# Performance work log

Measured on AMD Instinct MI355X. Metric: run time of the kernel, lower is better.

The kernel has to match this reference:

```python
import jax, jax.numpy as jnp
import numpy as np
import math

F = 64        # num_features (multiplicity of each irrep)
N = 16000     # nodes
E = 256000    # edges (avg_num_neighbors = 16)
S = 4         # num_species
DE = 32       # scalar edge feature dim (radial basis)
W = 128       # interaction_mlp_width
AVG_NEIGH = 16.0
SQ2 = math.sqrt(2.0)
SQ3 = math.sqrt(3.0)


def setup_inputs() -> dict:
    key = jax.random.key(0)
    ks = jax.random.split(key, 32)
    def nrm(k, shape, scale=1.0):
        return jax.random.normal(k, shape, dtype=jnp.float32) * scale
    inp = {}
    # forward args
    inp["vectors"] = nrm(ks[0], (E, 1, 3))
    inp["lengths"] = jax.random.uniform(ks[1], (E, 1), dtype=jnp.float32)
    inp["node_s"] = nrm(ks[2], (N, F))            # 64x0e part of node_feats
    inp["node_v"] = nrm(ks[3], (N, F, 3))         # 64x1o part of node_feats
    inp["scalar_edge_feats"] = nrm(ks[4], (E, DE))
    inp["node_specie"] = jax.random.randint(ks[5], (N,), 0, S)
    inp["senders"] = jax.random.randint(ks[6], (E,), 0, N)
    inp["receivers"] = jax.random.randint(ks[7], (E,), 0, N)
    # parameters (e3nn Linear = per-irrep channel mixing, fan-in normalized; bias only on 0e)
    inp["W_up_s"] = nrm(ks[8], (F, F), F ** -0.5); inp["b_up_s"] = jnp.zeros((F,), jnp.float32)
    inp["W_up_v"] = nrm(ks[9], (F, F), F ** -0.5)
    din = 2 * F + DE + 1
    inp["mlp_W1"] = nrm(ks[10], (din, W), din ** -0.5); inp["mlp_b1"] = jnp.zeros((W,), jnp.float32)
    inp["mlp_W2"] = nrm(ks[11], (W, W), W ** -0.5); inp["mlp_b2"] = jnp.zeros((W,), jnp.float32)
    inp["mlp_W3"] = nrm(ks[12], (W, 3 * F), W ** -0.5); inp["mlp_b3"] = jnp.zeros((3 * F,), jnp.float32)
    inp["W_dn_s"] = nrm(ks[13], (F, F), F ** -0.5); inp["b_dn_s"] = jnp.zeros((F,), jnp.float32)
    inp["W_dn_v"] = nrm(ks[14], (2 * F, F), (2 * F) ** -0.5)
    # symmetric contraction weights (per species, per channel); correlation=2
    inp["w_sc_s"] = nrm(ks[15], (S, 3, F), 3 ** -0.5)   # paths to 0e: x0, x0^2, (x1.x1)/sqrt3
    inp["w_sc_v"] = nrm(ks[16], (S, 2, F), 2 ** -0.5)   # paths to 1o: x1, x0*x1
    inp["W_pb_s"] = nrm(ks[17], (F, F), F ** -0.5); inp["b_pb_s"] = jnp.zeros((F,), jnp.float32)
    inp["W_pb_v"] = nrm(ks[18], (F, F), F ** -0.5)
    inp["W_r1_s"] = nrm(ks[19], (F, 2 * F), F ** -0.5); inp["b_r1_s"] = jnp.zeros((2 * F,), jnp.float32)
    inp["W_r1_v"] = nrm(ks[20], (F, F), F ** -0.5)
    inp["W_r2_s"] = nrm(ks[21], (F, 1), F ** -0.5); inp["b_r2"] = jnp.zeros((1,), jnp.float32)
    inp["W_r2_v"] = nrm(ks[22], (F, 1), F ** -0.5)
    return inp


def reference(vectors, lengths, node_s, node_v, scalar_edge_feats, node_specie,
              senders, receivers,
              W_up_s, b_up_s, W_up_v,
              mlp_W1, mlp_b1, mlp_W2, mlp_b2, mlp_W3, mlp_b3,
              W_dn_s, b_dn_s, W_dn_v,
              w_sc_s, w_sc_v, W_pb_s, b_pb_s, W_pb_v,
              W_r1_s, b_r1_s, W_r1_v, W_r2_s, b_r2, W_r2_v):
    n = node_s.shape[0]
    # --- spherical harmonics, sh_irreps='1o', component normalization, normalize=False ---
    edge_v = SQ3 * vectors[:, 0, :]                              # [E,3]

    # --- InteractionBlock: linear_up ---
    h_s = node_s @ W_up_s + b_up_s                               # [N,F]
    h_v = jnp.einsum('nfi,fg->ngi', node_v, W_up_v)              # [N,F,3]

    # --- MessagePassingConvolution ---
    m_s = h_s[senders]                                           # [E,F] 0e
    m_v = h_v[senders]                                           # [E,F,3] 1o
    # tensor product with edge 1o, filtered to 0e+1o (unitary CG):
    tp_s = jnp.einsum('efi,ei->ef', m_v, edge_v) / SQ3           # 1o x 1o -> 0e  [E,F]
    tp_v1 = m_s[:, :, None] * edge_v[:, None, :]                 # 0e x 1o -> 1o  [E,F,3]
    tp_v2 = jnp.cross(m_v, edge_v[:, None, :]) / SQ2             # 1o x 1o -> 1o  [E,F,3]
    # scalar MLP mix (one scalar weight per output irrep = 3F)
    mlp_in = jnp.concatenate([m_s, h_s[receivers], scalar_edge_feats, lengths], axis=1)
    h = jax.nn.silu(mlp_in @ mlp_W1 + mlp_b1)
    h = jax.nn.silu(h @ mlp_W2 + mlp_b2)
    mix = h @ mlp_W3 + mlp_b3                                    # [E,3F]
    mix_s, mix_v1, mix_v2 = mix[:, :F], mix[:, F:2 * F], mix[:, 2 * F:]
    tp_s = tp_s * mix_s
    tp_v = jnp.concatenate([tp_v1 * mix_v1[:, :, None], tp_v2 * mix_v2[:, :, None]], axis=1)  # [E,2F,3]
    # scatter-add to receivers, normalize by avg_num_neighbors
    agg_s = jax.ops.segment_sum(tp_s, receivers, num_segments=n) / AVG_NEIGH   # [N,F]
    agg_v = jax.ops.segment_sum(tp_v, receivers, num_segments=n) / AVG_NEIGH   # [N,2F,3]
    # linear_down
    f_s = agg_s @ W_dn_s + b_dn_s                                # [N,F]
    f_v = jnp.einsum('nfi,fg->ngi', agg_v, W_dn_v)               # [N,F,3]

    # --- EquivariantProductBasisBlock: symmetric contraction (correlation=2), per-species ---
    ws = w_sc_s[node_specie]                                     # [N,3,F]
    wv = w_sc_v[node_specie]                                     # [N,2,F]
    vv = jnp.sum(f_v * f_v, axis=-1) / SQ3                       # 1o (x) 1o -> 0e, symmetric
    sc_s = ws[:, 0] * f_s + ws[:, 1] * (f_s * f_s) + ws[:, 2] * vv           # [N,F]
    sc_v = wv[:, 0][:, :, None] * f_v + wv[:, 1][:, :, None] * (f_s[:, :, None] * f_v)  # [N,F,3]
    p_s = sc_s @ W_pb_s + b_pb_s                                 # node_feats 0e out
    p_v = jnp.einsum('nfi,fg->ngi', sc_v, W_pb_v)                # node_feats 1o out

    # --- NonLinearReadoutBlock: linear to (2F x 0e + F x 1o), gate, linear to 1x0e+1x1o ---
    r_s = p_s @ W_r1_s + b_r1_s                                  # [N,2F]
    r_v = jnp.einsum('nfi,fg->ngi', p_v, W_r1_v)                 # [N,F,3]
    act = jax.nn.silu(r_s[:, :F])
    gates = jax.nn.silu(r_s[:, F:])
    g_v = gates[:, :, None] * r_v                                # gated vectors
    out_s = act @ W_r2_s + b_r2                                  # [N,1]  0e output
    out_v = jnp.einsum('nfi,fo->noi', g_v, W_r2_v)               # [N,1,3] 1o output
    return out_s, out_v, p_s, p_v
```

## Files before the change

### kernel.cpp

```cpp
#include <hip/hip_runtime.h>

typedef short bf16x8 __attribute__((ext_vector_type(8)));
typedef float f32x4  __attribute__((ext_vector_type(4)));
typedef unsigned short ushort_t;

__device__ __forceinline__ float silu(float x) {
    float t = __expf(-x);
    return x * __builtin_amdgcn_rcpf(1.f + t);
}

__device__ __forceinline__ ushort_t f2bs(float x) {
    union { float f; unsigned int u; } v; v.f = x;
    unsigned int r = v.u + 0x7FFF + ((v.u >> 16) & 1);
    return (ushort_t)(r >> 16);
}
__device__ __forceinline__ ushort_t f2bs_t(float x) {
    union { float f; unsigned int u; } v; v.f = x;
    return (ushort_t)(v.u >> 16);
}
__device__ __forceinline__ float bs2f(ushort_t x) {
    union { unsigned int u; float f; } v; v.u = ((unsigned int)x) << 16; return v.f;
}

constexpr int N_   = 16000;
constexpr int E_   = 256000;
constexpr int Fd   = 64;

constexpr float SQ3f    = 1.7320508075688772f;
constexpr float INV_SQ3 = 0.5773502691896258f;
constexpr float INV_SQ2 = 0.7071067811865476f;
constexpr float INV_AVG = 0.0625f;

constexpr int OFF_OS = 0;
constexpr int OFF_OV = N_;
constexpr int OFF_PS = OFF_OV + 3 * N_;
constexpr int OFF_PV = OFF_PS + N_ * Fd;

constexpr int W1P_SZ = 6 * 8 * 512;
constexpr int W2P_SZ = 4 * 8 * 512;
constexpr int W3P_SZ = 4 * 12 * 512;

__global__ __launch_bounds__(256) void pack_kernel(
    const float* __restrict__ W1, const float* __restrict__ W2,
    const float* __restrict__ W3,
    ushort_t* __restrict__ W1p, ushort_t* __restrict__ W2p,
    ushort_t* __restrict__ W3p)
{
    int idx = blockIdx.x * 256 + threadIdx.x;
    if (idx < W1P_SZ) {
        int j = idx & 7, lane = (idx >> 3) & 63, tile = idx >> 9;
        int c = tile >> 3, t = tile & 7;
        int k = c * 32 + (lane >> 4) * 8 + j;
        int n = t * 16 + (lane & 15);
        W1p[idx] = f2bs(k < 161 ? W1[k * 128 + n] : 0.f);
    } else if (idx < W1P_SZ + W2P_SZ) {
        int q = idx - W1P_SZ;
        int j = q & 7, lane = (q >> 3) & 63, tile = q >> 9;
        int c = tile >> 3, t = tile & 7;
        int k = c * 32 + (lane >> 4) * 8 + j;
        int n = t * 16 + (lane & 15);
        W2p[q] = f2bs(W2[k * 128 + n]);
    } else {
        int q = idx - W1P_SZ - W2P_SZ;
        int j = q & 7, lane = (q >> 3) & 63, tile = q >> 9;
        int c = tile / 12, t = tile % 12;
        int k = c * 32 + (lane >> 4) * 8 + j;
        int n = t * 16 + (lane & 15);
        W3p[q] = f2bs(W3[k * 192 + n]);
    }
}

__global__ __launch_bounds__(64, 4) void up_kernel(
    const float* __restrict__ node_s, const float* __restrict__ node_v,
    const float* __restrict__ W_up_s, const float* __restrict__ b_up_s,
    const float* __restrict__ W_up_v,
    const int* __restrict__ receivers, int* __restrict__ cnt,
    ushort_t* __restrict__ hs_bf, float* __restrict__ h_v)
{
    __shared__ float ns[4][64];
    __shared__ float nv[4][64][3];
    const int n0 = blockIdx.x * 4;
    const int g  = threadIdx.x;

    {
        int e = blockIdx.x * 64 + g;
        atomicAdd(&cnt[receivers[e]], 1);
    }

    #pragma unroll
    for (int j = 0; j < 4; j++) ns[j][g] = node_s[(n0 + j) * 64 + g];
    for (int idx = g; idx < 4 * 192; idx += 64) {
        int j = idx / 192, r = idx - j * 192;
        nv[j][r / 3][r % 3] = node_v[(size_t)n0 * 192 + idx];
    }
    __syncthreads();

    float as[4], a0[4], a1[4], a2[4];
    float bb = b_up_s[g];
    #pragma unroll
    for (int j = 0; j < 4; j++) { as[j] = bb; a0[j] = a1[j] = a2[j] = 0.f; }
    #pragma unroll 4
    for (int f = 0; f < 64; f++) {
        float wss = W_up_s[f * 64 + g];
        float wv  = W_up_v[f * 64 + g];
        #pragma unroll
        for (int j = 0; j < 4; j++) {
            as[j] += ns[j][f] * wss;
            a0[j] += nv[j][f][0] * wv;
            a1[j] += nv[j][f][1] * wv;
            a2[j] += nv[j][f][2] * wv;
        }
    }
    #pragma unroll
    for (int j = 0; j < 4; j++) {
        hs_bf[(n0 + j) * 64 + g] = f2bs(as[j]);
        h_v[(n0 + j) * 192 + 0 * 64 + g] = a0[j];
        h_v[(n0 + j) * 192 + 1 * 64 + g] = a1[j];
        h_v[(n0 + j) * 192 + 2 * 64 + g] = a2[j];
    }
}

__global__ __launch_bounds__(1024) void scan_kernel(
    const int* __restrict__ cnt, int* __restrict__ base, int* __restrict__ cursor)
{
    __shared__ int part[1024];
    const int t = threadIdx.x;
    int v[16];
    int s = 0;
    if (t < 1000) {
        const int4* c4 = (const int4*)(cnt + t * 16);
        #pragma unroll
        for (int q = 0; q < 4; q++) {
            int4 w = c4[q];
            v[q * 4 + 0] = w.x; v[q * 4 + 1] = w.y;
            v[q * 4 + 2] = w.z; v[q * 4 + 3] = w.w;
            s += w.x + w.y + w.z + w.w;
        }
    }
    part[t] = s;
    __syncthreads();
    for (int off = 1; off < 1024; off <<= 1) {
        int u = (t >= off) ? part[t - off] : 0;
        __syncthreads();
        part[t] += u;
        __syncthreads();
    }
    if (t < 1000) {
        int run = part[t] - s;
        int b[16];
        #pragma unroll
        for (int i = 0; i < 16; i++) { b[i] = run; run += v[i]; }
        int4* bb = (int4*)(base + t * 16);
        int4* cc = (int4*)(cursor + t * 16);
        #pragma unroll
        for (int q = 0; q < 4; q++) {
            int4 w = { b[q * 4], b[q * 4 + 1], b[q * 4 + 2], b[q * 4 + 3] };
            bb[q] = w;
            cc[q] = w;
        }
    }
}

__global__ __launch_bounds__(128, 3) void edge_mlp_kernel(
    const float* __restrict__ lengths, const float* __restrict__ sef,
    const int* __restrict__ senders, const int* __restrict__ receivers,
    const float* __restrict__ b1f, const float* __restrict__ b2f,
    const float* __restrict__ b3f,
    const ushort_t* __restrict__ hs_bf,
    const ushort_t* __restrict__ W1p, const ushort_t* __restrict__ W2p,
    const ushort_t* __restrict__ W3p,
    int* __restrict__ cursor, int* __restrict__ sorted_eid,
    ushort_t* __restrict__ tpx)
{
    __shared__ ushort_t Hs[64 * 136];

    const int tid  = threadIdx.x;
    const int wave = tid >> 6, lane = tid & 63;
    const int quad = lane >> 4, l4 = lane & 15;
    const int ebase = blockIdx.x * 64 + wave * 32;
    const int me0   = ebase + l4;
    const int me1   = ebase + 16 + l4;
    const int hrow  = wave * 32;

    if (tid < 64) {
        int e = blockIdx.x * 64 + tid;
        int p = atomicAdd(&cursor[receivers[e]], 1);
        sorted_eid[p] = e;
    }

    const int snd0 = senders[me0], rcv0 = receivers[me0];
    const int snd1 = senders[me1], rcv1 = receivers[me1];

    bf16x8 a0[6], a1[6];
    a0[0] = *(const bf16x8*)(hs_bf + snd0 * 64 + quad * 8);
    a0[1] = *(const bf16x8*)(hs_bf + snd0 * 64 + 32 + quad * 8);
    a0[2] = *(const bf16x8*)(hs_bf + rcv0 * 64 + quad * 8);
    a0[3] = *(const bf16x8*)(hs_bf + rcv0 * 64 + 32 + quad * 8);
    a1[0] = *(const bf16x8*)(hs_bf + snd1 * 64 + quad * 8);
    a1[1] = *(const bf16x8*)(hs_bf + snd1 * 64 + 32 + quad * 8);
    a1[2] = *(const bf16x8*)(hs_bf + rcv1 * 64 + quad * 8);
    a1[3] = *(const bf16x8*)(hs_bf + rcv1 * 64 + 32 + quad * 8);
    {
        const float4 s0 = *(const float4*)(sef + (size_t)me0 * 32 + quad * 8);
        const float4 s1 = *(const float4*)(sef + (size_t)me0 * 32 + quad * 8 + 4);
        bf16x8 t;
        t[0] = (short)f2bs(s0.x); t[1] = (short)f2bs(s0.y);
        t[2] = (short)f2bs(s0.z); t[3] = (short)f2bs(s0.w);
        t[4] = (short)f2bs(s1.x); t[5] = (short)f2bs(s1.y);
        t[6] = (short)f2bs(s1.z); t[7] = (short)f2bs(s1.w);
        a0[4] = t;
        const float4 u0 = *(const float4*)(sef + (size_t)me1 * 32 + quad * 8);
        const float4 u1 = *(const float4*)(sef + (size_t)me1 * 32 + quad * 8 + 4);
        t[0] = (short)f2bs(u0.x); t[1] = (short)f2bs(u0.y);
        t[2] = (short)f2bs(u0.z); t[3] = (short)f2bs(u0.w);
        t[4] = (short)f2bs(u1.x); t[5] = (short)f2bs(u1.y);
        t[6] = (short)f2bs(u1.z); t[7] = (short)f2bs(u1.w);
        a1[4] = t;
    }
    {
        bf16x8 t = {0,0,0,0,0,0,0,0};
        bf16x8 u = {0,0,0,0,0,0,0,0};
        if (quad == 0) { t[0] = (short)f2bs(lengths[me0]); u[0] = (short)f2bs(lengths[me1]); }
        a0[5] = t; a1[5] = u;
    }

    const bf16x8* B1 = (const bf16x8*)W1p;
    const bf16x8* B2 = (const bf16x8*)W2p;
    const bf16x8* B3 = (const bf16x8*)W3p;

    f32x4 accA[8], accB[8];
    #pragma unroll
    for (int t = 0; t < 8; t++) { accA[t] = (f32x4){0,0,0,0}; accB[t] = (f32x4){0,0,0,0}; }
    #pragma unroll
    for (int c = 0; c < 6; c++) {
        #pragma unroll
        for (int t = 0; t < 8; t++) {
            bf16x8 b = B1[(c * 8 + t) * 64 + lane];
            accA[t] = __builtin_amdgcn_mfma_f32_16x16x32_bf16(a0[c], b, accA[t], 0, 0, 0);
            accB[t] = __builtin_amdgcn_mfma_f32_16x16x32_bf16(a1[c], b, accB[t], 0, 0, 0);
        }
    }
    #pragma unroll
    for (int t = 0; t < 8; t++) {
        float bb = b1f[t * 16 + l4];
        #pragma unroll
        for (int r = 0; r < 4; r++) {
            Hs[(hrow + quad * 4 + r) * 136 + t * 16 + l4]      = f2bs_t(silu(accA[t][r] + bb));
            Hs[(hrow + 16 + quad * 4 + r) * 136 + t * 16 + l4] = f2bs_t(silu(accB[t][r] + bb));
        }
    }

    #pragma unroll
    for (int t = 0; t < 8; t++) { accA[t] = (f32x4){0,0,0,0}; accB[t] = (f32x4){0,0,0,0}; }
    #pragma unroll
    for (int c = 0; c < 4; c++) {
        bf16x8 af0 = *(const bf16x8*)(&Hs[(hrow + l4) * 136 + c * 32 + quad * 8]);
        bf16x8 af1 = *(const bf16x8*)(&Hs[(hrow + 16 + l4) * 136 + c * 32 + quad * 8]);
        #pragma unroll
        for (int t = 0; t < 8; t++) {
            bf16x8 b = B2[(c * 8 + t) * 64 + lane];
            accA[t] = __builtin_amdgcn_mfma_f32_16x16x32_bf16(af0, b, accA[t], 0, 0, 0);
            accB[t] = __builtin_amdgcn_mfma_f32_16x16x32_bf16(af1, b, accB[t], 0, 0, 0);
        }
    }
    #pragma unroll
    for (int t = 0; t < 8; t++) {
        float bb = b2f[t * 16 + l4];
        #pragma unroll
        for (int r = 0; r < 4; r++) {
            Hs[(hrow + quad * 4 + r) * 136 + t * 16 + l4]      = f2bs_t(silu(accA[t][r] + bb));
            Hs[(hrow + 16 + quad * 4 + r) * 136 + t * 16 + l4] = f2bs_t(silu(accB[t][r] + bb));
        }
    }

    #pragma unroll
    for (int half = 0; half < 2; half++) {
        f32x4 acc3A[6], acc3B[6];
        #pragma unroll
        for (int t = 0; t < 6; t++) { acc3A[t] = (f32x4){0,0,0,0}; acc3B[t] = (f32x4){0,0,0,0}; }
        #pragma unroll
        for (int c = 0; c < 4; c++) {
            bf16x8 af0 = *(const bf16x8*)(&Hs[(hrow + l4) * 136 + c * 32 + quad * 8]);
            bf16x8 af1 = *(const bf16x8*)(&Hs[(hrow + 16 + l4) * 136 + c * 32 + quad * 8]);
            #pragma unroll
            for (int t = 0; t < 6; t++) {
                bf16x8 b = B3[(c * 12 + half * 6 + t) * 64 + lane];
                acc3A[t] = __builtin_amdgcn_mfma_f32_16x16x32_bf16(af0, b, acc3A[t], 0, 0, 0);
                acc3B[t] = __builtin_amdgcn_mfma_f32_16x16x32_bf16(af1, b, acc3B[t], 0, 0, 0);
            }
        }
        #pragma unroll
        for (int t = 0; t < 6; t++) {
            int tt = half * 6 + t;
            float bb = b3f[tt * 16 + l4];
            #pragma unroll
            for (int r = 0; r < 4; r++) {
                tpx[(size_t)(ebase + quad * 4 + r) * 192 + tt * 16 + l4]      = f2bs(acc3A[t][r] + bb);
                tpx[(size_t)(ebase + 16 + quad * 4 + r) * 192 + tt * 16 + l4] = f2bs(acc3B[t][r] + bb);
            }
        }
    }
}

__global__ __launch_bounds__(256, 2) void node_fused_kernel(
    const int* __restrict__ base, const int* __restrict__ cnt,
    const int* __restrict__ sorted_eid, const int* __restrict__ senders,
    const float* __restrict__ vectors,
    const ushort_t* __restrict__ tpx,
    const ushort_t* __restrict__ hs_bf, const float* __restrict__ h_v,
    const int* __restrict__ specie,
    const float* __restrict__ W_dn_s, const float* __restrict__ b_dn_s,
    const float* __restrict__ W_dn_v,
    const float* __restrict__ w_sc_s, const float* __restrict__ w_sc_v,
    const float* __restrict__ W_pb_s, const float* __restrict__ b_pb_s,
    const float* __restrict__ W_pb_v,
    const float* __restrict__ W_r1_s, const float* __restrict__ b_r1_s,
    const float* __restrict__ W_r1_v,
    const float* __restrict__ W_r2_s, const float* __restrict__ b_r2,
    const float* __restrict__ W_r2_v,
    float* __restrict__ out)
{
    __shared__ float as_l[4][64];
    __shared__ float av_l[4][128][3];
    __shared__ float scs[4][64];
    __shared__ float scv[4][64][3];
    __shared__ float ps_[4][64];
    __shared__ float pv_[4][64][3];
    __shared__ int   eids[4][64];

    const int tid = threadIdx.x;
    const int w   = tid >> 6;
    const int g   = tid & 63;
    const int n   = blockIdx.x * 4 + w;

    const int b = base[n];
    const int c = cnt[n];
    float accS = 0.f;
    float a10 = 0.f, a11 = 0.f, a12 = 0.f;
    float a20 = 0.f, a21 = 0.f, a22 = 0.f;

    for (int done = 0; done < c; done += 64) {
        int m = min(64, c - done);
        if (g < m) eids[w][g] = sorted_eid[b + done + g];
        for (int i = 0; i < m; i++) {
            const int e  = eids[w][i];
            const int se = senders[e];
            const float ev0 = SQ3f * vectors[e * 3 + 0];
            const float ev1 = SQ3f * vectors[e * 3 + 1];
            const float ev2 = SQ3f * vectors[e * 3 + 2];
            const float mv0 = h_v[(size_t)se * 192 + 0 * 64 + g];
            const float mv1 = h_v[(size_t)se * 192 + 1 * 64 + g];
            const float mv2 = h_v[(size_t)se * 192 + 2 * 64 + g];
            const float m_s = bs2f(hs_bf[se * 64 + g]);
            const ushort_t* mrow = tpx + (size_t)e * 192;
            const float c0 = bs2f(mrow[g]);
            const float c1 = bs2f(mrow[64 + g]);
            const float c2 = bs2f(mrow[128 + g]);

            float dot = mv0 * ev0 + mv1 * ev1 + mv2 * ev2;
            accS += dot * c0;
            float k1 = m_s * c1;
            a10 += k1 * ev0; a11 += k1 * ev1; a12 += k1 * ev2;
            a20 += (mv1 * ev2 - mv2 * ev1) * c2;
            a21 += (mv2 * ev0 - mv0 * ev2) * c2;
            a22 += (mv0 * ev1 - mv1 * ev0) * c2;
        }
    }
    as_l[w][g] = accS * (INV_SQ3 * INV_AVG);
    av_l[w][g][0] = a10 * INV_AVG;
    av_l[w][g][1] = a11 * INV_AVG;
    av_l[w][g][2] = a12 * INV_AVG;
    av_l[w][64 + g][0] = a20 * (INV_SQ2 * INV_AVG);
    av_l[w][64 + g][1] = a21 * (INV_SQ2 * INV_AVG);
    av_l[w][64 + g][2] = a22 * (INV_SQ2 * INV_AVG);

    float f_s = b_dn_s[g];
    #pragma unroll 8
    for (int f = 0; f < 64; f++) f_s += as_l[w][f] * W_dn_s[f * 64 + g];
    float fv0 = 0.f, fv1 = 0.f, fv2 = 0.f;
    #pragma unroll 8
    for (int f = 0; f < 128; f++) {
        float wt = W_dn_v[f * 64 + g];
        fv0 += av_l[w][f][0] * wt;
        fv1 += av_l[w][f][1] * wt;
        fv2 += av_l[w][f][2] * wt;
    }

    float vv = (fv0 * fv0 + fv1 * fv1 + fv2 * fv2) * INV_SQ3;
    int sp = specie[n];
    float ws0 = w_sc_s[sp * 192 + 0 * 64 + g];
    float ws1 = w_sc_s[sp * 192 + 1 * 64 + g];
    float ws2 = w_sc_s[sp * 192 + 2 * 64 + g];
    float wv0 = w_sc_v[sp * 128 + 0 * 64 + g];
    float wv1 = w_sc_v[sp * 128 + 1 * 64 + g];
    float sc_s = ws0 * f_s + ws1 * f_s * f_s + ws2 * vv;
    float kv = wv0 + wv1 * f_s;
    scs[w][g] = sc_s;
    scv[w][g][0] = kv * fv0;
    scv[w][g][1] = kv * fv1;
    scv[w][g][2] = kv * fv2;

    float p_s = b_pb_s[g];
    float pv0 = 0.f, pv1 = 0.f, pv2 = 0.f;
    #pragma unroll 8
    for (int f = 0; f < 64; f++) {
        float wps = W_pb_s[f * 64 + g];
        p_s += scs[w][f] * wps;
        float wpv = W_pb_v[f * 64 + g];
        pv0 += scv[w][f][0] * wpv;
        pv1 += scv[w][f][1] * wpv;
        pv2 += scv[w][f][2] * wpv;
    }
    ps_[w][g] = p_s;
    pv_[w][g][0] = pv0; pv_[w][g][1] = pv1; pv_[w][g][2] = pv2;

    out[OFF_PS + n * 64 + g] = p_s;
    out[OFF_PV + (size_t)n * 192 + g * 3 + 0] = pv0;
    out[OFF_PV + (size_t)n * 192 + g * 3 + 1] = pv1;
    out[OFF_PV + (size_t)n * 192 + g * 3 + 2] = pv2;

    float r0 = b_r1_s[g];
    float r1 = b_r1_s[g + 64];
    float rv0 = 0.f, rv1 = 0.f, rv2 = 0.f;
    #pragma unroll 8
    for (int f = 0; f < 64; f++) {
        float p = ps_[w][f];
        r0 += p * W_r1_s[f * 128 + g];
        r1 += p * W_r1_s[f * 128 + g + 64];
        float wrv = W_r1_v[f * 64 + g];
        rv0 += pv_[w][f][0] * wrv;
        rv1 += pv_[w][f][1] * wrv;
        rv2 += pv_[w][f][2] * wrv;
    }
    float act  = silu(r0);
    float gate = silu(r1);
    float o_s = act * W_r2_s[g];
    float wr2v = W_r2_v[g];
    float ov0 = gate * rv0 * wr2v;
    float ov1 = gate * rv1 * wr2v;
    float ov2 = gate * rv2 * wr2v;

    #pragma unroll
    for (int off = 32; off > 0; off >>= 1) {
        o_s += __shfl_down(o_s, off);
        ov0 += __shfl_down(ov0, off);
        ov1 += __shfl_down(ov1, off);
        ov2 += __shfl_down(ov2, off);
    }
    if (g == 0) {
        out[OFF_OS + n] = o_s + b_r2[0];
        out[OFF_OV + n * 3 + 0] = ov0;
        out[OFF_OV + n * 3 + 1] = ov1;
        out[OFF_OV + n * 3 + 2] = ov2;
    }
}

extern "C" void kernel_launch(void* const* d_in, const int* in_sizes, int n_in,
                              void* d_out, int out_size, void* d_ws, size_t ws_size,
                              hipStream_t stream)
{
    const float* vectors  = (const float*)d_in[0];
    const float* lengths  = (const float*)d_in[1];
    const float* node_s   = (const float*)d_in[2];
    const float* node_v   = (const float*)d_in[3];
    const float* sef      = (const float*)d_in[4];
    const int*  specie    = (const int*)d_in[5];
    const int*  senders   = (const int*)d_in[6];
    const int*  receivers = (const int*)d_in[7];
    const float* W_up_s   = (const float*)d_in[8];
    const float* b_up_s   = (const float*)d_in[9];
    const float* W_up_v   = (const float*)d_in[10];
    const float* mlp_W1   = (const float*)d_in[11];
    const float* mlp_b1   = (const float*)d_in[12];
    const float* mlp_W2   = (const float*)d_in[13];
    const float* mlp_b2   = (const float*)d_in[14];
    const float* mlp_W3   = (const float*)d_in[15];
    const float* mlp_b3   = (const float*)d_in[16];
    const float* W_dn_s   = (const float*)d_in[17];
    const float* b_dn_s   = (const float*)d_in[18];
    const float* W_dn_v   = (const float*)d_in[19];
    const float* w_sc_s   = (const float*)d_in[20];
    const float* w_sc_v   = (const float*)d_in[21];
    const float* W_pb_s   = (const float*)d_in[22];
    const float* b_pb_s   = (const float*)d_in[23];
    const float* W_pb_v   = (const float*)d_in[24];
    const float* W_r1_s   = (const float*)d_in[25];
    const float* b_r1_s   = (const float*)d_in[26];
    const float* W_r1_v   = (const float*)d_in[27];
    const float* W_r2_s   = (const float*)d_in[28];
    const float* b_r2     = (const float*)d_in[29];
    const float* W_r2_v   = (const float*)d_in[30];

    float* h_v = (float*)d_ws;
    ushort_t* tpx   = (ushort_t*)(h_v + (size_t)N_ * 192);
    ushort_t* hs_bf = tpx + (size_t)E_ * 192;
    ushort_t* W1p   = hs_bf + (size_t)N_ * 64;
    ushort_t* W2p   = W1p + W1P_SZ;
    ushort_t* W3p   = W2p + W2P_SZ;
    int* cnt        = (int*)((((size_t)(W3p + W3P_SZ)) + 15) & ~(size_t)15);
    int* base       = cnt + N_;
    int* cursor     = base + N_;
    int* sorted_eid = cursor + N_;

    float* out = (float*)d_out;

    hipMemsetAsync(cnt, 0, N_ * sizeof(int), stream);

    up_kernel<<<N_ / 4, 64, 0, stream>>>(node_s, node_v, W_up_s, b_up_s, W_up_v,
                                         receivers, cnt, hs_bf, h_v);
    pack_kernel<<<256, 256, 0, stream>>>(mlp_W1, mlp_W2, mlp_W3, W1p, W2p, W3p);
    scan_kernel<<<1, 1024, 0, stream>>>(cnt, base, cursor);

    edge_mlp_kernel<<<E_ / 64, 128, 0, stream>>>(
        lengths, sef, senders, receivers,
        mlp_b1, mlp_b2, mlp_b3,
        hs_bf, W1p, W2p, W3p, cursor, sorted_eid, tpx);

    node_fused_kernel<<<N_ / 4, 256, 0, stream>>>(
        base, cnt, sorted_eid, senders, vectors,
        tpx, hs_bf, h_v, specie,
        W_dn_s, b_dn_s, W_dn_v, w_sc_s, w_sc_v,
        W_pb_s, b_pb_s, W_pb_v, W_r1_s, b_r1_s, W_r1_v,
        W_r2_s, b_r2, W_r2_v, out);
}
```

Measured before the change: 424.9 us.

## Stage edge MLP inputs in LDS, split output tiles across four waves, unroll node gather

```diff
diff --git a/kernel.cpp b/kernel.cpp
--- a/kernel.cpp
+++ b/kernel.cpp
@@ -161,7 +161,7 @@
     }
 }
 
-__global__ __launch_bounds__(128, 3) void edge_mlp_kernel(
+__global__ __launch_bounds__(256, 3) void edge_mlp_kernel(
     const float* __restrict__ lengths, const float* __restrict__ sef,
     const int* __restrict__ senders, const int* __restrict__ receivers,
     const float* __restrict__ b1f, const float* __restrict__ b2f,
@@ -172,132 +172,144 @@
     int* __restrict__ cursor, int* __restrict__ sorted_eid,
     ushort_t* __restrict__ tpx)
 {
+    __shared__ ushort_t Als[64 * 200];
     __shared__ ushort_t Hs[64 * 136];
 
     const int tid  = threadIdx.x;
     const int wave = tid >> 6, lane = tid & 63;
     const int quad = lane >> 4, l4 = lane & 15;
-    const int ebase = blockIdx.x * 64 + wave * 32;
-    const int me0   = ebase + l4;
-    const int me1   = ebase + 16 + l4;
-    const int hrow  = wave * 32;
+    const int e0   = blockIdx.x * 64;
 
     if (tid < 64) {
-        int e = blockIdx.x * 64 + tid;
+        int e = e0 + tid;
         int p = atomicAdd(&cursor[receivers[e]], 1);
         sorted_eid[p] = e;
     }
 
-    const int snd0 = senders[me0], rcv0 = receivers[me0];
-    const int snd1 = senders[me1], rcv1 = receivers[me1];
-
-    bf16x8 a0[6], a1[6];
-    a0[0] = *(const bf16x8*)(hs_bf + snd0 * 64 + quad * 8);
-    a0[1] = *(const bf16x8*)(hs_bf + snd0 * 64 + 32 + quad * 8);
-    a0[2] = *(const bf16x8*)(hs_bf + rcv0 * 64 + quad * 8);
-    a0[3] = *(const bf16x8*)(hs_bf + rcv0 * 64 + 32 + quad * 8);
-    a1[0] = *(const bf16x8*)(hs_bf + snd1 * 64 + quad * 8);
-    a1[1] = *(const bf16x8*)(hs_bf + snd1 * 64 + 32 + quad * 8);
-    a1[2] = *(const bf16x8*)(hs_bf + rcv1 * 64 + quad * 8);
-    a1[3] = *(const bf16x8*)(hs_bf + rcv1 * 64 + 32 + quad * 8);
     {
-        const float4 s0 = *(const float4*)(sef + (size_t)me0 * 32 + quad * 8);
-        const float4 s1 = *(const float4*)(sef + (size_t)me0 * 32 + quad * 8 + 4);
-        bf16x8 t;
-        t[0] = (short)f2bs(s0.x); t[1] = (short)f2bs(s0.y);
-        t[2] = (short)f2bs(s0.z); t[3] = (short)f2bs(s0.w);
-        t[4] = (short)f2bs(s1.x); t[5] = (short)f2bs(s1.y);
-        t[6] = (short)f2bs(s1.z); t[7] = (short)f2bs(s1.w);
-        a0[4] = t;
-        const float4 u0 = *(const float4*)(sef + (size_t)me1 * 32 + quad * 8);
-        const float4 u1 = *(const float4*)(sef + (size_t)me1 * 32 + quad * 8 + 4);
-        t[0] = (short)f2bs(u0.x); t[1] = (short)f2bs(u0.y);
-        t[2] = (short)f2bs(u0.z); t[3] = (short)f2bs(u0.w);
-        t[4] = (short)f2bs(u1.x); t[5] = (short)f2bs(u1.y);
-        t[6] = (short)f2bs(u1.z); t[7] = (short)f2bs(u1.w);
-        a1[4] = t;
-    }
-    {
-        bf16x8 t = {0,0,0,0,0,0,0,0};
-        bf16x8 u = {0,0,0,0,0,0,0,0};
-        if (quad == 0) { t[0] = (short)f2bs(lengths[me0]); u[0] = (short)f2bs(lengths[me1]); }
-        a0[5] = t; a1[5] = u;
-    }
+        const int e  = tid & 63;
+        const int ge = e0 + e;
+        const int snd = senders[ge];
+        const int rcv = receivers[ge];
+        for (int c = tid >> 6; c < 24; c += 4) {
+            bf16x8 v;
+            if (c < 8) {
+                v = *(const bf16x8*)(hs_bf + snd * 64 + c * 8);
+            } else if (c < 16) {
+                v = *(const bf16x8*)(hs_bf + rcv * 64 + (c - 8) * 8);
+            } else if (c < 20) {
+                const float4 s0 = *(const float4*)(sef + (size_t)ge * 32 + (c - 16) * 8);
+                const float4 s1 = *(const float4*)(sef + (size_t)ge * 32 + (c - 16) * 8 + 4);
+                v[0] = (short)f2bs(s0.x); v[1] = (short)f2bs(s0.y);
+                v[2] = (short)f2bs(s0.z); v[3] = (short)f2bs(s0.w);
+                v[4] = (short)f2bs(s1.x); v[5] = (short)f2bs(s1.y);
+                v[6] = (short)f2bs(s1.z); v[7] = (short)f2bs(s1.w);
+            } else if (c == 20) {
+                v = (bf16x8){0,0,0,0,0,0,0,0};
+                v[0] = (short)f2bs(lengths[ge]);
+            } else {
+                v = (bf16x8){0,0,0,0,0,0,0,0};
+            }
+            *(bf16x8*)(&Als[e * 200 + c * 8]) = v;
+        }
+    }
+    __syncthreads();
 
     const bf16x8* B1 = (const bf16x8*)W1p;
     const bf16x8* B2 = (const bf16x8*)W2p;
     const bf16x8* B3 = (const bf16x8*)W3p;
 
-    f32x4 accA[8], accB[8];
-    #pragma unroll
-    for (int t = 0; t < 8; t++) { accA[t] = (f32x4){0,0,0,0}; accB[t] = (f32x4){0,0,0,0}; }
-    #pragma unroll
-    for (int c = 0; c < 6; c++) {
-        #pragma unroll
-        for (int t = 0; t < 8; t++) {
-            bf16x8 b = B1[(c * 8 + t) * 64 + lane];
-            accA[t] = __builtin_amdgcn_mfma_f32_16x16x32_bf16(a0[c], b, accA[t], 0, 0, 0);
-            accB[t] = __builtin_amdgcn_mfma_f32_16x16x32_bf16(a1[c], b, accB[t], 0, 0, 0);
-        }
-    }
-    #pragma unroll
-    for (int t = 0; t < 8; t++) {
-        float bb = b1f[t * 16 + l4];
-        #pragma unroll
-        for (int r = 0; r < 4; r++) {
-            Hs[(hrow + quad * 4 + r) * 136 + t * 16 + l4]      = f2bs_t(silu(accA[t][r] + bb));
-            Hs[(hrow + 16 + quad * 4 + r) * 136 + t * 16 + l4] = f2bs_t(silu(accB[t][r] + bb));
-        }
-    }
-
-    #pragma unroll
-    for (int t = 0; t < 8; t++) { accA[t] = (f32x4){0,0,0,0}; accB[t] = (f32x4){0,0,0,0}; }
-    #pragma unroll
-    for (int c = 0; c < 4; c++) {
-        bf16x8 af0 = *(const bf16x8*)(&Hs[(hrow + l4) * 136 + c * 32 + quad * 8]);
-        bf16x8 af1 = *(const bf16x8*)(&Hs[(hrow + 16 + l4) * 136 + c * 32 + quad * 8]);
-        #pragma unroll
-        for (int t = 0; t < 8; t++) {
-            bf16x8 b = B2[(c * 8 + t) * 64 + lane];
-            accA[t] = __builtin_amdgcn_mfma_f32_16x16x32_bf16(af0, b, accA[t], 0, 0, 0);
-            accB[t] = __builtin_amdgcn_mfma_f32_16x16x32_bf16(af1, b, accB[t], 0, 0, 0);
-        }
-    }
-    #pragma unroll
-    for (int t = 0; t < 8; t++) {
-        float bb = b2f[t * 16 + l4];
-        #pragma unroll
-        for (int r = 0; r < 4; r++) {
-            Hs[(hrow + quad * 4 + r) * 136 + t * 16 + l4]      = f2bs_t(silu(accA[t][r] + bb));
-            Hs[(hrow + 16 + quad * 4 + r) * 136 + t * 16 + l4] = f2bs_t(silu(accB[t][r] + bb));
-        }
-    }
-
-    #pragma unroll
-    for (int half = 0; half < 2; half++) {
-        f32x4 acc3A[6], acc3B[6];
-        #pragma unroll
-        for (int t = 0; t < 6; t++) { acc3A[t] = (f32x4){0,0,0,0}; acc3B[t] = (f32x4){0,0,0,0}; }
+    {
+        f32x4 acc[2][4];
+        #pragma unroll
+        for (int ti = 0; ti < 2; ti++)
+            #pragma unroll
+            for (int m = 0; m < 4; m++) acc[ti][m] = (f32x4){0,0,0,0};
+        #pragma unroll
+        for (int c = 0; c < 6; c++) {
+            bf16x8 b0 = B1[(c * 8 + wave * 2 + 0) * 64 + lane];
+            bf16x8 b1 = B1[(c * 8 + wave * 2 + 1) * 64 + lane];
+            #pragma unroll
+            for (int m = 0; m < 4; m++) {
+                bf16x8 a = *(const bf16x8*)(&Als[(m * 16 + l4) * 200 + c * 32 + quad * 8]);
+                acc[0][m] = __builtin_amdgcn_mfma_f32_16x16x32_bf16(a, b0, acc[0][m], 0, 0, 0);
+                acc[1][m] = __builtin_amdgcn_mfma_f32_16x16x32_bf16(a, b1, acc[1][m], 0, 0, 0);
+            }
+        }
+        #pragma unroll
+        for (int ti = 0; ti < 2; ti++) {
+            int t = wave * 2 + ti;
+            float bb = b1f[t * 16 + l4];
+            #pragma unroll
+            for (int m = 0; m < 4; m++)
+                #pragma unroll
+                for (int r = 0; r < 4; r++)
+                    Hs[(m * 16 + quad * 4 + r) * 136 + t * 16 + l4] =
+                        f2bs_t(silu(acc[ti][m][r] + bb));
+        }
+    }
+    __syncthreads();
+
+    {
+        f32x4 acc[2][4];
+        #pragma unroll
+        for (int ti = 0; ti < 2; ti++)
+            #pragma unroll
+            for (int m = 0; m < 4; m++) acc[ti][m] = (f32x4){0,0,0,0};
         #pragma unroll
         for (int c = 0; c < 4; c++) {
-            bf16x8 af0 = *(const bf16x8*)(&Hs[(hrow + l4) * 136 + c * 32 + quad * 8]);
-            bf16x8 af1 = *(const bf16x8*)(&Hs[(hrow + 16 + l4) * 136 + c * 32 + quad * 8]);
-            #pragma unroll
-            for (int t = 0; t < 6; t++) {
-                bf16x8 b = B3[(c * 12 + half * 6 + t) * 64 + lane];
-                acc3A[t] = __builtin_amdgcn_mfma_f32_16x16x32_bf16(af0, b, acc3A[t], 0, 0, 0);
-                acc3B[t] = __builtin_amdgcn_mfma_f32_16x16x32_bf16(af1, b, acc3B[t], 0, 0, 0);
+            bf16x8 b0 = B2[(c * 8 + wave * 2 + 0) * 64 + lane];
+            bf16x8 b1 = B2[(c * 8 + wave * 2 + 1) * 64 + lane];
+            #pragma unroll
+            for (int m = 0; m < 4; m++) {
+                bf16x8 a = *(const bf16x8*)(&Hs[(m * 16 + l4) * 136 + c * 32 + quad * 8]);
+                acc[0][m] = __builtin_amdgcn_mfma_f32_16x16x32_bf16(a, b0, acc[0][m], 0, 0, 0);
+                acc[1][m] = __builtin_amdgcn_mfma_f32_16x16x32_bf16(a, b1, acc[1][m], 0, 0, 0);
             }
         }
         #pragma unroll
-        for (int t = 0; t < 6; t++) {
-            int tt = half * 6 + t;
-            float bb = b3f[tt * 16 + l4];
-            #pragma unroll
-            for (int r = 0; r < 4; r++) {
-                tpx[(size_t)(ebase + quad * 4 + r) * 192 + tt * 16 + l4]      = f2bs(acc3A[t][r] + bb);
-                tpx[(size_t)(ebase + 16 + quad * 4 + r) * 192 + tt * 16 + l4] = f2bs(acc3B[t][r] + bb);
+        for (int ti = 0; ti < 2; ti++) {
+            int t = wave * 2 + ti;
+            float bb = b2f[t * 16 + l4];
+            #pragma unroll
+            for (int m = 0; m < 4; m++)
+                #pragma unroll
+                for (int r = 0; r < 4; r++)
+                    Als[(m * 16 + quad * 4 + r) * 136 + t * 16 + l4] =
+                        f2bs_t(silu(acc[ti][m][r] + bb));
+        }
+    }
+    __syncthreads();
+
+    {
+        f32x4 acc[3][4];
+        #pragma unroll
+        for (int ti = 0; ti < 3; ti++)
+            #pragma unroll
+            for (int m = 0; m < 4; m++) acc[ti][m] = (f32x4){0,0,0,0};
+        #pragma unroll
+        for (int c = 0; c < 4; c++) {
+            bf16x8 b0 = B3[(c * 12 + wave * 3 + 0) * 64 + lane];
+            bf16x8 b1 = B3[(c * 12 + wave * 3 + 1) * 64 + lane];
+            bf16x8 b2 = B3[(c * 12 + wave * 3 + 2) * 64 + lane];
+            #pragma unroll
+            for (int m = 0; m < 4; m++) {
+                bf16x8 a = *(const bf16x8*)(&Als[(m * 16 + l4) * 136 + c * 32 + quad * 8]);
+                acc[0][m] = __builtin_amdgcn_mfma_f32_16x16x32_bf16(a, b0, acc[0][m], 0, 0, 0);
+                acc[1][m] = __builtin_amdgcn_mfma_f32_16x16x32_bf16(a, b1, acc[1][m], 0, 0, 0);
+                acc[2][m] = __builtin_amdgcn_mfma_f32_16x16x32_bf16(a, b2, acc[2][m], 0, 0, 0);
             }
+        }
+        #pragma unroll
+        for (int ti = 0; ti < 3; ti++) {
+            int t = wave * 3 + ti;
+            float bb = b3f[t * 16 + l4];
+            #pragma unroll
+            for (int m = 0; m < 4; m++)
+                #pragma unroll
+                for (int r = 0; r < 4; r++)
+                    tpx[(size_t)(e0 + m * 16 + quad * 4 + r) * 192 + t * 16 + l4] =
+                        f2bs(acc[ti][m][r] + bb);
         }
     }
 }
@@ -335,44 +347,79 @@
 
     const int b = base[n];
     const int c = cnt[n];
-    float accS = 0.f;
-    float a10 = 0.f, a11 = 0.f, a12 = 0.f;
-    float a20 = 0.f, a21 = 0.f, a22 = 0.f;
+    float accSa = 0.f, accSb = 0.f;
+    float a10a = 0.f, a11a = 0.f, a12a = 0.f;
+    float a20a = 0.f, a21a = 0.f, a22a = 0.f;
+    float a10b = 0.f, a11b = 0.f, a12b = 0.f;
+    float a20b = 0.f, a21b = 0.f, a22b = 0.f;
 
     for (int done = 0; done < c; done += 64) {
         int m = min(64, c - done);
         if (g < m) eids[w][g] = sorted_eid[b + done + g];
-        for (int i = 0; i < m; i++) {
-            const int e  = eids[w][i];
-            const int se = senders[e];
-            const float ev0 = SQ3f * vectors[e * 3 + 0];
-            const float ev1 = SQ3f * vectors[e * 3 + 1];
-            const float ev2 = SQ3f * vectors[e * 3 + 2];
-            const float mv0 = h_v[(size_t)se * 192 + 0 * 64 + g];
-            const float mv1 = h_v[(size_t)se * 192 + 1 * 64 + g];
-            const float mv2 = h_v[(size_t)se * 192 + 2 * 64 + g];
-            const float m_s = bs2f(hs_bf[se * 64 + g]);
-            const ushort_t* mrow = tpx + (size_t)e * 192;
-            const float c0 = bs2f(mrow[g]);
-            const float c1 = bs2f(mrow[64 + g]);
-            const float c2 = bs2f(mrow[128 + g]);
-
-            float dot = mv0 * ev0 + mv1 * ev1 + mv2 * ev2;
-            accS += dot * c0;
-            float k1 = m_s * c1;
-            a10 += k1 * ev0; a11 += k1 * ev1; a12 += k1 * ev2;
-            a20 += (mv1 * ev2 - mv2 * ev1) * c2;
-            a21 += (mv2 * ev0 - mv0 * ev2) * c2;
-            a22 += (mv0 * ev1 - mv1 * ev0) * c2;
-        }
-    }
-    as_l[w][g] = accS * (INV_SQ3 * INV_AVG);
-    av_l[w][g][0] = a10 * INV_AVG;
-    av_l[w][g][1] = a11 * INV_AVG;
-    av_l[w][g][2] = a12 * INV_AVG;
-    av_l[w][64 + g][0] = a20 * (INV_SQ2 * INV_AVG);
-    av_l[w][64 + g][1] = a21 * (INV_SQ2 * INV_AVG);
-    av_l[w][64 + g][2] = a22 * (INV_SQ2 * INV_AVG);
+        int i = 0;
+        for (; i + 1 < m; i += 2) {
+            const int e1 = eids[w][i];
+            const int e2 = eids[w][i + 1];
+            const int se1 = senders[e1];
+            const int se2 = senders[e2];
+            const float ev10 = SQ3f * vectors[e1 * 3 + 0];
+            const float ev11 = SQ3f * vectors[e1 * 3 + 1];
+            const float ev12 = SQ3f * vectors[e1 * 3 + 2];
+            const float ev20 = SQ3f * vectors[e2 * 3 + 0];
+            const float ev21 = SQ3f * vectors[e2 * 3 + 1];
+            const float ev22 = SQ3f * vectors[e2 * 3 + 2];
+            const float m10 = h_v[(size_t)se1 * 192 + 0 * 64 + g];
+            const float m11 = h_v[(size_t)se1 * 192 + 1 * 64 + g];
+            const float m12 = h_v[(size_t)se1 * 192 + 2 * 64 + g];
+            const float m20 = h_v[(size_t)se2 * 192 + 0 * 64 + g];
+            const float m21 = h_v[(size_t)se2 * 192 + 1 * 64 + g];
+            const float m22 = h_v[(size_t)se2 * 192 + 2 * 64 + g];
+            const float ms1 = bs2f(hs_bf[se1 * 64 + g]);
+            const float ms2 = bs2f(hs_bf[se2 * 64 + g]);
+            const ushort_t* r1 = tpx + (size_t)e1 * 192;
+            const ushort_t* r2 = tpx + (size_t)e2 * 192;
+            const float c10 = bs2f(r1[g]), c11 = bs2f(r1[64 + g]), c12 = bs2f(r1[128 + g]);
+            const float c20 = bs2f(r2[g]), c21 = bs2f(r2[64 + g]), c22 = bs2f(r2[128 + g]);
+
+            accSa += (m10 * ev10 + m11 * ev11 + m12 * ev12) * c10;
+            accSb += (m20 * ev20 + m21 * ev21 + m22 * ev22) * c20;
+            float k1a = ms1 * c11, k1b = ms2 * c21;
+            a10a += k1a * ev10; a11a += k1a * ev11; a12a += k1a * ev12;
+            a10b += k1b * ev20; a11b += k1b * ev21; a12b += k1b * ev22;
+            a20a += (m11 * ev12 - m12 * ev11) * c12;
+            a21a += (m12 * ev10 - m10 * ev12) * c12;
+            a22a += (m10 * ev11 - m11 * ev10) * c12;
+            a20b += (m21 * ev22 - m22 * ev21) * c22;
+            a21b += (m22 * ev20 - m20 * ev22) * c22;
+            a22b += (m20 * ev21 - m21 * ev20) * c22;
+        }
+        if (i < m) {
+            const int e1 = eids[w][i];
+            const int se1 = senders[e1];
+            const float ev10 = SQ3f * vectors[e1 * 3 + 0];
+            const float ev11 = SQ3f * vectors[e1 * 3 + 1];
+            const float ev12 = SQ3f * vectors[e1 * 3 + 2];
+            const float m10 = h_v[(size_t)se1 * 192 + 0 * 64 + g];
+            const float m11 = h_v[(size_t)se1 * 192 + 1 * 64 + g];
+            const float m12 = h_v[(size_t)se1 * 192 + 2 * 64 + g];
+            const float ms1 = bs2f(hs_bf[se1 * 64 + g]);
+            const ushort_t* r1 = tpx + (size_t)e1 * 192;
+            const float c10 = bs2f(r1[g]), c11 = bs2f(r1[64 + g]), c12 = bs2f(r1[128 + g]);
+            accSa += (m10 * ev10 + m11 * ev11 + m12 * ev12) * c10;
+            float k1a = ms1 * c11;
+            a10a += k1a * ev10; a11a += k1a * ev11; a12a += k1a * ev12;
+            a20a += (m11 * ev12 - m12 * ev11) * c12;
+            a21a += (m12 * ev10 - m10 * ev12) * c12;
+            a22a += (m10 * ev11 - m11 * ev10) * c12;
+        }
+    }
+    as_l[w][g] = (accSa + accSb) * (INV_SQ3 * INV_AVG);
+    av_l[w][g][0] = (a10a + a10b) * INV_AVG;
+    av_l[w][g][1] = (a11a + a11b) * INV_AVG;
+    av_l[w][g][2] = (a12a + a12b) * INV_AVG;
+    av_l[w][64 + g][0] = (a20a + a20b) * (INV_SQ2 * INV_AVG);
+    av_l[w][64 + g][1] = (a21a + a21b) * (INV_SQ2 * INV_AVG);
+    av_l[w][64 + g][2] = (a22a + a22b) * (INV_SQ2 * INV_AVG);
 
     float f_s = b_dn_s[g];
     #pragma unroll 8
@@ -511,7 +558,7 @@
     pack_kernel<<<256, 256, 0, stream>>>(mlp_W1, mlp_W2, mlp_W3, W1p, W2p, W3p);
     scan_kernel<<<1, 1024, 0, stream>>>(cnt, base, cursor);
 
-    edge_mlp_kernel<<<E_ / 64, 128, 0, stream>>>(
+    edge_mlp_kernel<<<E_ / 64, 256, 0, stream>>>(
         lengths, sef, senders, receivers,
         mlp_b1, mlp_b2, mlp_b3,
         hs_bf, W1p, W2p, W3p, cursor, sorted_eid, tpx);
```

Measured after the change: 364.4 us. 1.17x faster.
